# Performance work log

Hardware: AMD Instinct MI355X
Metric: run time of the kernel (lower is better)

The kernel has to match this reference:

```python
import jax, jax.numpy as jnp
import numpy as np

V = 6890      # FAUST vertex count (also n_classes)
R, A = 5, 8   # radial / angular template discretization
C_IN = 544    # SHOT descriptor dim
DIMS = [96, 128, 128]  # isc_layer_dims


def setup_inputs() -> dict:
    key = jax.random.key(0)
    ks = jax.random.split(key, 12)
    signal = jax.random.normal(ks[0], (V, C_IN), jnp.float32)
    bc_idx = jax.random.randint(ks[1], (V, R, A, 3), 0, V, jnp.int32)
    w = jax.random.uniform(ks[2], (V, R, A, 3), jnp.float32)
    bc_w = w / jnp.sum(w, axis=-1, keepdims=True)  # barycentric weights sum to 1
    c_ins = [C_IN] + DIMS[:-1]
    params = {}
    for i, (t, c) in enumerate(zip(DIMS, c_ins)):
        params[f"t{i}"] = jax.random.normal(ks[3 + 2 * i], (t, R, A, c), jnp.float32) * 0.05
        params[f"b{i}"] = jnp.zeros((t,), jnp.float32)
    Wd = jax.random.normal(ks[10], (DIMS[-1], V), jnp.float32) * 0.05
    bd = jnp.zeros((V,), jnp.float32)
    return {"signal": signal, "bc_idx": bc_idx, "bc_w": bc_w, **params, "Wd": Wd, "bd": bd}


def _conv_dirac_amp(sig, idx, w, T, b):
    # barycentric interpolation of the signal at template vertices:
    # gather sig[idx] -> [V,R,A,3,C], weight-sum over the 3 corners -> [V,R,A,C]
    interp = jnp.einsum('vrai,vraic->vrac', w, sig[idx])
    # template matching for every angular rotation (rotation_delta=1 -> A rotations)
    outs = [jnp.einsum('vrac,trac->vt', jnp.roll(interp, -o, axis=2), T) for o in range(A)]
    x = jax.nn.relu(jnp.stack(outs, axis=1) + b)  # [V, A_rot, T]
    # AngularMaxPooling: max over rotation axis
    return jnp.max(x, axis=1)  # [V, T]


def reference(signal, bc_idx, bc_w, t0, b0, t1, b1, t2, b2, Wd, bd):
    x = signal
    for T, b in ((t0, b0), (t1, b1), (t2, b2)):
        x = _conv_dirac_amp(x, bc_idx, bc_w, T, b)
    return x @ Wd + bd  # [V, 6890] per-vertex class logits
```

## Files before the change

kernel.cpp:

```cpp
#include <hip/hip_runtime.h>

typedef unsigned short u16;
typedef unsigned int   u32;
typedef __bf16 bf16x8 __attribute__((ext_vector_type(8)));
typedef float  f32x4  __attribute__((ext_vector_type(4)));
typedef u32    u32x4  __attribute__((ext_vector_type(4)));
typedef u32    u32x2  __attribute__((ext_vector_type(2)));
typedef u16    u16x4  __attribute__((ext_vector_type(4)));

#define V_N   6890
#define V_PAD 6912
#define SQ2H  0.70710678118654752f

__device__ __forceinline__ float bf2f(u32 h) {
  union { u32 u; float f; } c; c.u = h << 16; return c.f;
}
__device__ __forceinline__ u16 f2bf(float f) {
  union { float f; u32 u; } c; c.f = f;
  return (u16)((c.u + 0x7fffu + ((c.u >> 16) & 1u)) >> 16);
}
__device__ __forceinline__ u32 pk(float lo, float hi) {
  return (u32)f2bf(lo) | ((u32)f2bf(hi) << 16);
}
__device__ __forceinline__ void gload_lds16(const void* g, void* l) {
  __builtin_amdgcn_global_load_lds((const __attribute__((address_space(1))) void*)g,
                                   (__attribute__((address_space(3))) void*)l, 16, 0, 0);
}

__device__ __forceinline__ void rfft8(const float* x, float& Z0, float& Re1, float& Im1,
                                      float& Re2, float& Im2, float& Re3, float& Im3, float& Z4) {
  float s04 = x[0] + x[4], d04 = x[0] - x[4];
  float s26 = x[2] + x[6], d26 = x[2] - x[6];
  float s15 = x[1] + x[5], d15 = x[1] - x[5];
  float s37 = x[3] + x[7], d37 = x[3] - x[7];
  float e = s04 + s26, f = s15 + s37;
  Z0 = e + f; Z4 = e - f;
  Re2 = s04 - s26; Im2 = s37 - s15;
  float t1 = SQ2H * (d15 - d37), t2 = SQ2H * (d15 + d37);
  Re1 = d04 + t1; Re3 = d04 - t1;
  Im1 = -(t2 + d26); Im3 = d26 - t2;
}

__global__ void cvt_kernel(const float* __restrict__ in, u16* __restrict__ out, int total4) {
  int g = blockIdx.x * 256 + threadIdx.x;
  if (g >= total4) return;
  f32x4 v = *(const f32x4*)(in + (size_t)g * 4);
  u16x4 o; o.x = f2bf(v.x); o.y = f2bf(v.y); o.z = f2bf(v.z); o.w = f2bf(v.w);
  *(u16x4*)(out + (size_t)g * 4) = o;
}

__global__ void trot_fft_kernel(const float* __restrict__ T, u16* __restrict__ B,
                                int Tn, int Cc, int C4, int K0pad, int K1, int total) {
  int g = blockIdx.x * 256 + threadIdx.x;
  if (g >= total) return;
  int c4 = g % C4; int q = g / C4;
  int r = q % 5; int t = q / 5;
  float hs[8][4];
#pragma unroll
  for (int a = 0; a < 8; ++a) {
    f32x4 va = *(const f32x4*)(T + ((size_t)((t * 5 + r) * 8 + a)) * Cc + c4 * 4);
#pragma unroll
    for (int j = 0; j < 4; ++j) hs[a][j] = va[j];
  }
  float Z0[4], Z4[4], Re[3][4], Im[3][4];
#pragma unroll
  for (int ch = 0; ch < 4; ++ch) {
    float x[8];
#pragma unroll
    for (int a = 0; a < 8; ++a) x[a] = hs[a][ch];
    float z0, r1, i1, r2, i2, r3, i3, z4;
    rfft8(x, z0, r1, i1, r2, i2, r3, i3, z4);
    Z0[ch] = z0 * 0.125f; Z4[ch] = z4 * 0.125f;
    Re[0][ch] = r1 * 0.25f; Im[0][ch] = i1 * 0.25f;
    Re[1][ch] = r2 * 0.25f; Im[1][ch] = i2 * 0.25f;
    Re[2][ch] = r3 * 0.25f; Im[2][ch] = i3 * 0.25f;
  }
  int cb = c4 * 4;
  u32x2 w0v; w0v[0] = pk(Z0[0], Z0[1]); w0v[1] = pk(Z0[2], Z0[3]);
  *(u32x2*)(B + (size_t)t * K0pad + r * Cc + cb) = w0v;
  size_t bo1 = (size_t)Tn * K0pad;
  size_t binSz = (size_t)2 * Tn * K1;
  int off = ((r * Cc + cb) << 1);
#pragma unroll
  for (int k = 0; k < 3; ++k) {
    u32x4 wr, wi;
#pragma unroll
    for (int j = 0; j < 4; ++j) {
      wr[j] = pk(Re[k][j], Im[k][j]);
      wi[j] = pk(-Im[k][j], Re[k][j]);
    }
    *(u32x4*)(B + bo1 + k * binSz + (size_t)t * K1 + off) = wr;
    *(u32x4*)(B + bo1 + k * binSz + (size_t)(Tn + t) * K1 + off) = wi;
  }
  u32x2 w4v; w4v[0] = pk(Z4[0], Z4[1]); w4v[1] = pk(Z4[2], Z4[3]);
  *(u32x2*)(B + bo1 + 3 * binSz + (size_t)t * K0pad + r * Cc + cb) = w4v;
}

__global__ void bpad_kernel(u16* __restrict__ B, int K0pad, int pad, size_t b4off, int total) {
  int g = blockIdx.x * 256 + threadIdx.x;
  if (g >= total) return;
  int p = g % pad; int t = g / pad;
  size_t o = (size_t)t * K0pad + (K0pad - pad) + p;
  B[o] = 0;
  B[b4off + o] = 0;
}

__global__ void interp_fft_kernel(const u16* __restrict__ sig, int Cc, int C8,
                                  const int* __restrict__ idx, const float* __restrict__ wgt,
                                  u16* __restrict__ out, int v0, int Kpad, int K0pad, int K1,
                                  int total) {
  int g = blockIdx.x * 256 + threadIdx.x;
  if (g >= total) return;
  int c8 = g % C8; int q = g / C8;
  int r = q % 5; int vr = q / 5;
  size_t ib = ((size_t)((v0 + vr) * 5 + r)) * 24;
  float xs[8][8];
#pragma unroll
  for (int a = 0; a < 8; ++a) {
    int i0 = idx[ib + a * 3], i1 = idx[ib + a * 3 + 1], i2 = idx[ib + a * 3 + 2];
    float w0 = wgt[ib + a * 3], w1 = wgt[ib + a * 3 + 1], w2 = wgt[ib + a * 3 + 2];
    u32x4 s0 = *(const u32x4*)(sig + (size_t)i0 * Cc + c8 * 8);
    u32x4 s1 = *(const u32x4*)(sig + (size_t)i1 * Cc + c8 * 8);
    u32x4 s2 = *(const u32x4*)(sig + (size_t)i2 * Cc + c8 * 8);
#pragma unroll
    for (int j = 0; j < 4; ++j) {
      xs[a][2 * j]     = w0 * bf2f(s0[j] & 0xffffu) + w1 * bf2f(s1[j] & 0xffffu) + w2 * bf2f(s2[j] & 0xffffu);
      xs[a][2 * j + 1] = w0 * bf2f(s0[j] >> 16)     + w1 * bf2f(s1[j] >> 16)     + w2 * bf2f(s2[j] >> 16);
    }
  }
  float Z0[8], Z4[8], Re1[8], Im1[8], Re2[8], Im2[8], Re3[8], Im3[8];
#pragma unroll
  for (int ch = 0; ch < 8; ++ch) {
    float x[8];
#pragma unroll
    for (int a = 0; a < 8; ++a) x[a] = xs[a][ch];
    rfft8(x, Z0[ch], Re1[ch], Im1[ch], Re2[ch], Im2[ch], Re3[ch], Im3[ch], Z4[ch]);
  }
  size_t rowb = (size_t)vr * Kpad;
  int cb = c8 * 8;
  u32x4 a0, a4;
#pragma unroll
  for (int p = 0; p < 4; ++p) {
    a0[p] = pk(Z0[2 * p], Z0[2 * p + 1]);
    a4[p] = pk(Z4[2 * p], Z4[2 * p + 1]);
  }
  *(u32x4*)(out + rowb + r * Cc + cb) = a0;
  *(u32x4*)(out + rowb + K0pad + 3 * K1 + r * Cc + cb) = a4;
  int off1 = K0pad + ((r * Cc + cb) << 1);
  u32x4 wa, wb;
#pragma unroll
  for (int j = 0; j < 4; ++j) { wa[j] = pk(Re1[j], Im1[j]); wb[j] = pk(Re1[4 + j], Im1[4 + j]); }
  *(u32x4*)(out + rowb + off1) = wa;
  *(u32x4*)(out + rowb + off1 + 8) = wb;
#pragma unroll
  for (int j = 0; j < 4; ++j) { wa[j] = pk(Re2[j], Im2[j]); wb[j] = pk(Re2[4 + j], Im2[4 + j]); }
  *(u32x4*)(out + rowb + off1 + K1) = wa;
  *(u32x4*)(out + rowb + off1 + K1 + 8) = wb;
#pragma unroll
  for (int j = 0; j < 4; ++j) { wa[j] = pk(Re3[j], Im3[j]); wb[j] = pk(Re3[4 + j], Im3[4 + j]); }
  *(u32x4*)(out + rowb + off1 + 2 * K1) = wa;
  *(u32x4*)(out + rowb + off1 + 2 * K1 + 8) = wb;
}

__global__ void amp_fft(const float* __restrict__ Cin, size_t cstride,
                        const float* __restrict__ bias, u16* __restrict__ out,
                        int Tn, int ldo, int split,
                        int ns0, int ns1, int ns2, int ns3, int ns4, int total) {
  int g = blockIdx.x * 256 + threadIdx.x;
  if (g >= total) return;
  int t = g % Tn, v = g / Tn;
  const int nsA[8] = {ns0, ns1, ns1, ns2, ns2, ns3, ns3, ns4};
  float sec[8];
  size_t base = (size_t)v * (8 * Tn) + t;
#pragma unroll
  for (int s = 0; s < 8; ++s) {
    const float* p = Cin + base + s * Tn;
    float a = p[0];
    for (int k = 1; k < nsA[s]; ++k) a += p[(size_t)k * cstride];
    sec[s] = a;
  }
  const float Ct[8] = {1.f, SQ2H, 0.f, -SQ2H, -1.f, -SQ2H, 0.f, SQ2H};
  const float St[8] = {0.f, SQ2H, 1.f, SQ2H, 0.f, -SQ2H, -1.f, -SQ2H};
  float m;
#pragma unroll
  for (int o = 0; o < 8; ++o) {
    float val = sec[0] + ((o & 1) ? -sec[7] : sec[7])
      + sec[1] * Ct[o]           - sec[2] * St[o]
      + sec[3] * Ct[(2 * o) & 7] - sec[4] * St[(2 * o) & 7]
      + sec[5] * Ct[(3 * o) & 7] - sec[6] * St[(3 * o) & 7];
    m = (o == 0) ? val : fmaxf(m, val);
  }
  m = fmaxf(m + bias[t], 0.f);
  u16 hi = f2bf(m);
  out[(size_t)v * ldo + t] = hi;
  if (split) out[(size_t)v * ldo + Tn + t] = f2bf(m - bf2f(hi));
}

__global__ void wdt_kernel(const float* __restrict__ Wd, u16* __restrict__ out, int total) {
  int g = blockIdx.x * 256 + threadIdx.x;
  if (g >= total) return;
  int k = g & 127, n = g >> 7;
  float v = (n < V_N) ? Wd[(size_t)k * V_N + n] : 0.f;
  u16 hi = f2bf(v);
  out[(size_t)n * 256 + k] = hi;
  out[(size_t)n * 256 + 128 + k] = f2bf(v - bf2f(hi));
}

struct GTab {
  int start[6];
  int aOff[5];
  int bOff[5];
  int cOff[5];
  int Kg[5];
  int kch[5];
  int ntn[5];
  int Nv[5];
};

__global__ __launch_bounds__(512, 2) void gemm_grp(
    const u16* __restrict__ A, int lda, const u16* __restrict__ Bbase,
    float* __restrict__ C, int ldc, size_t cstride,
    const float* __restrict__ bias, int Mvalid, int ntm, int nG, GTab tb) {
  __shared__ __align__(16) u16 lA[2][256 * 64];
  __shared__ __align__(16) u16 lB[2][256 * 64];
  const int tid = threadIdx.x;
  const int w = tid >> 6, l = tid & 63;

  const int nb = gridDim.x, bid = blockIdx.x;
  const int qq = nb >> 3, rr = nb & 7;
  const int xcd = bid & 7, ii = bid >> 3;
  const int vb = (xcd < rr ? xcd * (qq + 1) : rr * (qq + 1) + (xcd - rr) * qq) + ii;

  int gI = 0;
#pragma unroll
  for (int k = 1; k < 5; ++k) if (k < nG && vb >= tb.start[k]) gI = k;
  const int local = vb - tb.start[gI];
  const int ntnG = tb.ntn[gI];
  const int per = ntm * ntnG;
  const int s = local / per;
  const int rem = local - s * per;
  const int tm = rem / ntnG, tn = rem - tm * ntnG;
  const int Kg = tb.Kg[gI];
  const int kb = s * tb.kch[gI];
  int ke = kb + tb.kch[gI]; if (ke > Kg) ke = Kg;
  const int nt = (ke - kb + 63) >> 6;
  const int Nv = tb.Nv[gI];
  const int cO = tb.cOff[gI];
  const int ldb = Kg;
  float* Cb = C + (size_t)s * cstride;

  const u16* Ab = A + (size_t)(tm * 256) * lda + tb.aOff[gI] + kb;
  const u16* Bb = Bbase + tb.bOff[gI] + (size_t)(tn * 256) * ldb + kb;

  const int srow = tid >> 3;
  const int scol = (((l & 7) ^ (srow & 7)) << 3);
  u16* laBase = &lA[0][0];
  u16* lbBase = &lB[0][0];

  auto STAGE = [&](int buf, int k0) {
    const u16* ga = Ab + (size_t)srow * lda + k0 + scol;
    const u16* gb = Bb + (size_t)srow * ldb + k0 + scol;
    u16* la = laBase + buf * (256 * 64) + w * 512;
    u16* lb = lbBase + buf * (256 * 64) + w * 512;
#pragma unroll
    for (int i = 0; i < 4; ++i) {
      gload_lds16(ga + (size_t)(i * 64) * lda, la + i * 4096);
      gload_lds16(gb + (size_t)(i * 64) * ldb, lb + i * 4096);
    }
  };

  f32x4 acc[8][4];
#pragma unroll
  for (int i = 0; i < 8; ++i)
#pragma unroll
    for (int j = 0; j < 4; ++j) acc[i][j] = (f32x4){0.f, 0.f, 0.f, 0.f};

  const int wm = w >> 2, wn = w & 3;
  const int aoffbase = (wm * 128 + (l & 15)) * 64;
  const int boffbase = (wn * 64 + (l & 15)) * 64;
  const int ksel = l >> 4, swz = l & 7;
  const int kc0 = ((ksel ^ swz) << 3);
  const int kc1 = (((4 + ksel) ^ swz) << 3);

  STAGE(0, 0);
  int cur = 0;
  for (int t = 0; t < nt; ++t) {
    if (t + 1 < nt) STAGE(cur ^ 1, (t + 1) * 64);
    __builtin_amdgcn_sched_barrier(0);
    if (t + 1 < nt) { asm volatile("s_waitcnt vmcnt(8)" ::: "memory"); }
    else            { asm volatile("s_waitcnt vmcnt(0)" ::: "memory"); }
    __builtin_amdgcn_s_barrier();
    __builtin_amdgcn_sched_barrier(0);
    const u16* lab = laBase + cur * (256 * 64);
    const u16* lbb = lbBase + cur * (256 * 64);
#pragma unroll
    for (int kk = 0; kk < 2; ++kk) {
      const int kc = kk ? kc1 : kc0;
      bf16x8 bfr[4];
#pragma unroll
      for (int ni = 0; ni < 4; ++ni)
        bfr[ni] = *(const bf16x8*)&lbb[boffbase + ni * 1024 + kc];
#pragma unroll
      for (int mh = 0; mh < 2; ++mh) {
        bf16x8 afr[4];
#pragma unroll
        for (int mi = 0; mi < 4; ++mi)
          afr[mi] = *(const bf16x8*)&lab[aoffbase + (mh * 4 + mi) * 1024 + kc];
        __builtin_amdgcn_s_setprio(1);
#pragma unroll
        for (int mi = 0; mi < 4; ++mi)
#pragma unroll
          for (int ni = 0; ni < 4; ++ni)
            acc[mh * 4 + mi][ni] =
                __builtin_amdgcn_mfma_f32_16x16x32_bf16(afr[mi], bfr[ni], acc[mh * 4 + mi][ni], 0, 0, 0);
        __builtin_amdgcn_s_setprio(0);
      }
    }
    __builtin_amdgcn_sched_barrier(0);
    __builtin_amdgcn_s_barrier();
    cur ^= 1;
  }

  const int row0 = tm * 256 + wm * 128 + ((l >> 4) << 2);
  const int col0 = tn * 256 + wn * 64 + (l & 15);
#pragma unroll
  for (int mi = 0; mi < 8; ++mi) {
#pragma unroll
    for (int j = 0; j < 4; ++j) {
      int grow = row0 + mi * 16 + j;
      if (grow < Mvalid) {
#pragma unroll
        for (int ni = 0; ni < 4; ++ni) {
          int gcol = col0 + ni * 16;
          if (gcol < Nv) {
            float vv = acc[mi][ni][j];
            int gc = cO + gcol;
            if (bias) vv += bias[gc];
            Cb[(size_t)grow * ldc + gc] = vv;
          }
        }
      }
    }
  }
}

static inline int imin(int a, int b) { return a < b ? a : b; }

extern "C" void kernel_launch(void* const* d_in, const int* in_sizes, int n_in,
                              void* d_out, int out_size, void* d_ws, size_t ws_size,
                              hipStream_t stream) {
  const float* signal = (const float*)d_in[0];
  const int*   bc_idx = (const int*)d_in[1];
  const float* bc_w   = (const float*)d_in[2];
  const float* tmpl[3] = { (const float*)d_in[3], (const float*)d_in[5], (const float*)d_in[7] };
  const float* tb[3]   = { (const float*)d_in[4], (const float*)d_in[6], (const float*)d_in[8] };
  const float* Wd = (const float*)d_in[9];
  const float* bd = (const float*)d_in[10];
  float* outp = (float*)d_out;

  char* ws = (char*)d_ws;
  size_t off = 0;
  auto alloc = [&](size_t b) -> void* {
    size_t o = (off + 255) & ~(size_t)255; off = o + b; return (void*)(ws + o);
  };
  u16* sigbf = (u16*)alloc((size_t)V_N * 544 * 2);
  u16* outL0 = (u16*)alloc((size_t)V_PAD * 96 * 2);
  u16* outL1 = (u16*)alloc((size_t)V_PAD * 128 * 2);
  u16* outL2 = (u16*)alloc((size_t)V_PAD * 256 * 2);
  u16* trot  = (u16*)alloc((size_t)8 * 1024 * 1024 * 2);
  float* gemmC = (float*)alloc((size_t)4 * V_PAD * 1024 * 4);
  size_t o2 = (off + 255) & ~(size_t)255;
  u16* interp = (u16*)(ws + o2);
  size_t interpElems = (ws_size > o2) ? (ws_size - o2) / 2 : 0;

  { int total4 = V_N * 544 / 4;
    cvt_kernel<<<dim3((total4 + 255) / 256), dim3(256), 0, stream>>>(signal, sigbf, total4); }

  const int TnA[3] = {96, 128, 128}, CcA[3] = {544, 96, 128};
  const int nsTab[3][5] = {{2,5,5,4,2},{3,4,4,4,3},{3,4,4,4,3}};
  const int CrA[3] = {3584, V_PAD, V_PAD};
  u16* outs[3] = { outL0, outL1, outL2 };
  const u16* cursig = sigbf;
  for (int L = 0; L < 3; ++L) {
    const int Tn = TnA[L], Cc = CcA[L];
    const int C8 = Cc / 8, C4 = Cc / 4;
    const int K0 = 5 * Cc, K0pad = ((K0 + 63) / 64) * 64;
    const int K1 = 10 * Cc;
    const int Kpad = 2 * K0pad + 3 * K1;
    const int N = 8 * Tn;
    const int* ns = nsTab[L];
    const size_t cstride = (size_t)V_PAD * N;

    { int total = Tn * 5 * C4;
      trot_fft_kernel<<<dim3((total + 255) / 256), dim3(256), 0, stream>>>(
          tmpl[L], trot, Tn, Cc, C4, K0pad, K1, total); }
    int pad = K0pad - K0;
    if (pad > 0) {
      int total = Tn * pad;
      size_t b4off = (size_t)Tn * K0pad + (size_t)6 * Tn * K1;
      bpad_kernel<<<dim3((total + 255) / 256), dim3(256), 0, stream>>>(trot, K0pad, pad, b4off, total);
    }

    GTab tg;
    int Kg5[5] = {K0pad, K1, K1, K1, K0pad};
    int Ng5[5] = {Tn, 2 * Tn, 2 * Tn, 2 * Tn, Tn};
    tg.aOff[0] = 0; tg.aOff[1] = K0pad; tg.aOff[2] = K0pad + K1;
    tg.aOff[3] = K0pad + 2 * K1; tg.aOff[4] = K0pad + 3 * K1;
    tg.bOff[0] = 0; tg.bOff[1] = Tn * K0pad;
    tg.bOff[2] = Tn * K0pad + 2 * Tn * K1;
    tg.bOff[3] = Tn * K0pad + 4 * Tn * K1;
    tg.bOff[4] = Tn * K0pad + 6 * Tn * K1;
    tg.cOff[0] = 0; tg.cOff[1] = Tn; tg.cOff[2] = 3 * Tn; tg.cOff[3] = 5 * Tn; tg.cOff[4] = 7 * Tn;
    for (int g5 = 0; g5 < 5; ++g5) {
      tg.Kg[g5] = Kg5[g5];
      tg.kch[g5] = ((Kg5[g5] / 64 + ns[g5] - 1) / ns[g5]) * 64;
      tg.ntn[g5] = 1;
      tg.Nv[g5] = Ng5[g5];
    }

    long crl = (long)(interpElems / (size_t)Kpad) & ~(long)255;
    int cr = (crl > (long)CrA[L]) ? CrA[L] : (int)crl;
    if (cr < 256) cr = 256;
    for (int v0 = 0; v0 < V_PAD; v0 += cr) {
      int rows = imin(cr, V_PAD - v0);
      int nv = imin(rows, V_N - v0);
      { int total = nv * 5 * C8;
        interp_fft_kernel<<<dim3((total + 255) / 256), dim3(256), 0, stream>>>(
            cursig, Cc, C8, bc_idx, bc_w, interp, v0, Kpad, K0pad, K1, total); }
      int ntm = rows / 256;
      tg.start[0] = 0;
      for (int g5 = 0; g5 < 5; ++g5) tg.start[g5 + 1] = tg.start[g5] + ns[g5] * ntm;
      gemm_grp<<<dim3(tg.start[5]), dim3(512), 0, stream>>>(
          interp, Kpad, trot, gemmC + (size_t)v0 * N, N, cstride, nullptr, nv, ntm, 5, tg);
    }
    { int total = V_N * Tn;
      int ldo = (L == 2) ? 256 : ((L == 0) ? 96 : 128);
      amp_fft<<<dim3((total + 255) / 256), dim3(256), 0, stream>>>(
          gemmC, cstride, tb[L], outs[L], Tn, ldo, (L == 2) ? 1 : 0,
          ns[0], ns[1], ns[2], ns[3], ns[4], total); }
    cursig = outs[L];
  }

  { int total = V_PAD * 128;
    wdt_kernel<<<dim3((total + 255) / 256), dim3(256), 0, stream>>>(Wd, trot, total); }
  GTab td;
  td.start[0] = 0; td.start[1] = 27 * 27;
  td.aOff[0] = 0; td.bOff[0] = 0; td.cOff[0] = 0;
  td.Kg[0] = 256; td.kch[0] = 256; td.ntn[0] = 27; td.Nv[0] = V_N;
  for (int g5 = 1; g5 < 5; ++g5) { td.start[g5 + 1] = td.start[1]; td.aOff[g5] = 0; td.bOff[g5] = 0;
    td.cOff[g5] = 0; td.Kg[g5] = 256; td.kch[g5] = 256; td.ntn[g5] = 1; td.Nv[g5] = 0; }
  gemm_grp<<<dim3(27 * 27), dim3(512), 0, stream>>>(
      outL2, 256, trot, outp, V_N, 0, bd, V_N, 27, 1, td);
}
```

Baseline: 637.8 us.

## Add half-width N tile for real-bin GEMM groups, cut split-K, fuse pad kernel

Adds a 256x128 tile variant to the grouped GEMM for the DC and Nyquist bins, whose N is only Tn (96 or 128), so half of the old 256-wide B tile is no longer wasted. The split-K factors for layers 1 and 2 are lowered, which reduces partial-sum output traffic and the reduction work in amp_fft. The bpad zeroing kernel is folded into the trot FFT kernel to save one launch per layer. In exchange there are fewer blocks in layers 1 and 2 and more branching in the GEMM kernel, which may raise register pressure.

```diff
diff --git a/kernel.cpp b/kernel.cpp
--- a/kernel.cpp
+++ b/kernel.cpp
@@ -50,9 +50,18 @@
 }
 
 __global__ void trot_fft_kernel(const float* __restrict__ T, u16* __restrict__ B,
-                                int Tn, int Cc, int C4, int K0pad, int K1, int total) {
+                                int Tn, int Cc, int C4, int K0pad, int K1, int total, int pad) {
   int g = blockIdx.x * 256 + threadIdx.x;
-  if (g >= total) return;
+  if (g >= total) {
+    int g2 = g - total;
+    int padTot = Tn * pad;
+    if (g2 >= padTot) return;
+    int p = g2 % pad; int t = g2 / pad;
+    size_t b4off = (size_t)Tn * K0pad + (size_t)6 * Tn * K1;
+    size_t o = (size_t)t * K0pad + (K0pad - pad) + p;
+    B[o] = 0; B[b4off + o] = 0;
+    return;
+  }
   int c4 = g % C4; int q = g / C4;
   int r = q % 5; int t = q / 5;
   float hs[8][4];
@@ -94,15 +103,6 @@
   }
   u32x2 w4v; w4v[0] = pk(Z4[0], Z4[1]); w4v[1] = pk(Z4[2], Z4[3]);
   *(u32x2*)(B + bo1 + 3 * binSz + (size_t)t * K0pad + r * Cc + cb) = w4v;
-}
-
-__global__ void bpad_kernel(u16* __restrict__ B, int K0pad, int pad, size_t b4off, int total) {
-  int g = blockIdx.x * 256 + threadIdx.x;
-  if (g >= total) return;
-  int p = g % pad; int t = g / pad;
-  size_t o = (size_t)t * K0pad + (K0pad - pad) + p;
-  B[o] = 0;
-  B[b4off + o] = 0;
 }
 
 __global__ void interp_fft_kernel(const u16* __restrict__ sig, int Cc, int C8,
@@ -215,6 +215,7 @@
   int kch[5];
   int ntn[5];
   int Nv[5];
+  int nh[5];
 };
 
 __global__ __launch_bounds__(512, 2) void gemm_grp(
@@ -246,97 +247,170 @@
   const int nt = (ke - kb + 63) >> 6;
   const int Nv = tb.Nv[gI];
   const int cO = tb.cOff[gI];
+  const int nh = tb.nh[gI];
   const int ldb = Kg;
   float* Cb = C + (size_t)s * cstride;
 
   const u16* Ab = A + (size_t)(tm * 256) * lda + tb.aOff[gI] + kb;
-  const u16* Bb = Bbase + tb.bOff[gI] + (size_t)(tn * 256) * ldb + kb;
+  const u16* Bb = Bbase + tb.bOff[gI] + (size_t)(tn * (nh ? 128 : 256)) * ldb + kb;
 
   const int srow = tid >> 3;
   const int scol = (((l & 7) ^ (srow & 7)) << 3);
   u16* laBase = &lA[0][0];
   u16* lbBase = &lB[0][0];
 
-  auto STAGE = [&](int buf, int k0) {
-    const u16* ga = Ab + (size_t)srow * lda + k0 + scol;
-    const u16* gb = Bb + (size_t)srow * ldb + k0 + scol;
-    u16* la = laBase + buf * (256 * 64) + w * 512;
-    u16* lb = lbBase + buf * (256 * 64) + w * 512;
-#pragma unroll
-    for (int i = 0; i < 4; ++i) {
-      gload_lds16(ga + (size_t)(i * 64) * lda, la + i * 4096);
-      gload_lds16(gb + (size_t)(i * 64) * ldb, lb + i * 4096);
-    }
-  };
-
   f32x4 acc[8][4];
 #pragma unroll
   for (int i = 0; i < 8; ++i)
 #pragma unroll
     for (int j = 0; j < 4; ++j) acc[i][j] = (f32x4){0.f, 0.f, 0.f, 0.f};
 
-  const int wm = w >> 2, wn = w & 3;
-  const int aoffbase = (wm * 128 + (l & 15)) * 64;
-  const int boffbase = (wn * 64 + (l & 15)) * 64;
   const int ksel = l >> 4, swz = l & 7;
   const int kc0 = ((ksel ^ swz) << 3);
   const int kc1 = (((4 + ksel) ^ swz) << 3);
 
-  STAGE(0, 0);
-  int cur = 0;
-  for (int t = 0; t < nt; ++t) {
-    if (t + 1 < nt) STAGE(cur ^ 1, (t + 1) * 64);
-    __builtin_amdgcn_sched_barrier(0);
-    if (t + 1 < nt) { asm volatile("s_waitcnt vmcnt(8)" ::: "memory"); }
-    else            { asm volatile("s_waitcnt vmcnt(0)" ::: "memory"); }
-    __builtin_amdgcn_s_barrier();
-    __builtin_amdgcn_sched_barrier(0);
-    const u16* lab = laBase + cur * (256 * 64);
-    const u16* lbb = lbBase + cur * (256 * 64);
-#pragma unroll
-    for (int kk = 0; kk < 2; ++kk) {
-      const int kc = kk ? kc1 : kc0;
-      bf16x8 bfr[4];
-#pragma unroll
-      for (int ni = 0; ni < 4; ++ni)
-        bfr[ni] = *(const bf16x8*)&lbb[boffbase + ni * 1024 + kc];
-#pragma unroll
-      for (int mh = 0; mh < 2; ++mh) {
+  if (nh) {
+    const int wm = w >> 1, wn = w & 1;
+    const int aoffbase = (wm * 64 + (l & 15)) * 64;
+    const int boffbase = (wn * 64 + (l & 15)) * 64;
+    auto STAGE = [&](int buf, int k0) {
+      const u16* ga = Ab + (size_t)srow * lda + k0 + scol;
+      const u16* gb = Bb + (size_t)srow * ldb + k0 + scol;
+      u16* la = laBase + buf * (256 * 64) + w * 512;
+      u16* lb = lbBase + buf * (256 * 64) + w * 512;
+#pragma unroll
+      for (int i = 0; i < 4; ++i)
+        gload_lds16(ga + (size_t)(i * 64) * lda, la + i * 4096);
+#pragma unroll
+      for (int i = 0; i < 2; ++i)
+        gload_lds16(gb + (size_t)(i * 64) * ldb, lb + i * 4096);
+    };
+    STAGE(0, 0);
+    int cur = 0;
+    for (int t = 0; t < nt; ++t) {
+      if (t + 1 < nt) STAGE(cur ^ 1, (t + 1) * 64);
+      __builtin_amdgcn_sched_barrier(0);
+      if (t + 1 < nt) { asm volatile("s_waitcnt vmcnt(6)" ::: "memory"); }
+      else            { asm volatile("s_waitcnt vmcnt(0)" ::: "memory"); }
+      __builtin_amdgcn_s_barrier();
+      __builtin_amdgcn_sched_barrier(0);
+      const u16* lab = laBase + cur * (256 * 64);
+      const u16* lbb = lbBase + cur * (256 * 64);
+#pragma unroll
+      for (int kk = 0; kk < 2; ++kk) {
+        const int kc = kk ? kc1 : kc0;
+        bf16x8 bfr[4];
+#pragma unroll
+        for (int ni = 0; ni < 4; ++ni)
+          bfr[ni] = *(const bf16x8*)&lbb[boffbase + ni * 1024 + kc];
         bf16x8 afr[4];
 #pragma unroll
         for (int mi = 0; mi < 4; ++mi)
-          afr[mi] = *(const bf16x8*)&lab[aoffbase + (mh * 4 + mi) * 1024 + kc];
+          afr[mi] = *(const bf16x8*)&lab[aoffbase + mi * 1024 + kc];
         __builtin_amdgcn_s_setprio(1);
 #pragma unroll
         for (int mi = 0; mi < 4; ++mi)
 #pragma unroll
           for (int ni = 0; ni < 4; ++ni)
-            acc[mh * 4 + mi][ni] =
-                __builtin_amdgcn_mfma_f32_16x16x32_bf16(afr[mi], bfr[ni], acc[mh * 4 + mi][ni], 0, 0, 0);
+            acc[mi][ni] =
+                __builtin_amdgcn_mfma_f32_16x16x32_bf16(afr[mi], bfr[ni], acc[mi][ni], 0, 0, 0);
         __builtin_amdgcn_s_setprio(0);
       }
-    }
-    __builtin_amdgcn_sched_barrier(0);
-    __builtin_amdgcn_s_barrier();
-    cur ^= 1;
-  }
-
-  const int row0 = tm * 256 + wm * 128 + ((l >> 4) << 2);
-  const int col0 = tn * 256 + wn * 64 + (l & 15);
-#pragma unroll
-  for (int mi = 0; mi < 8; ++mi) {
-#pragma unroll
-    for (int j = 0; j < 4; ++j) {
-      int grow = row0 + mi * 16 + j;
-      if (grow < Mvalid) {
-#pragma unroll
-        for (int ni = 0; ni < 4; ++ni) {
-          int gcol = col0 + ni * 16;
-          if (gcol < Nv) {
-            float vv = acc[mi][ni][j];
-            int gc = cO + gcol;
-            if (bias) vv += bias[gc];
-            Cb[(size_t)grow * ldc + gc] = vv;
+      __builtin_amdgcn_sched_barrier(0);
+      __builtin_amdgcn_s_barrier();
+      cur ^= 1;
+    }
+    const int row0 = tm * 256 + wm * 64 + ((l >> 4) << 2);
+    const int col0 = tn * 128 + wn * 64 + (l & 15);
+#pragma unroll
+    for (int mi = 0; mi < 4; ++mi) {
+#pragma unroll
+      for (int j = 0; j < 4; ++j) {
+        int grow = row0 + mi * 16 + j;
+        if (grow < Mvalid) {
+#pragma unroll
+          for (int ni = 0; ni < 4; ++ni) {
+            int gcol = col0 + ni * 16;
+            if (gcol < Nv) {
+              float vv = acc[mi][ni][j];
+              int gc = cO + gcol;
+              if (bias) vv += bias[gc];
+              Cb[(size_t)grow * ldc + gc] = vv;
+            }
+          }
+        }
+      }
+    }
+  } else {
+    const int wm = w >> 2, wn = w & 3;
+    const int aoffbase = (wm * 128 + (l & 15)) * 64;
+    const int boffbase = (wn * 64 + (l & 15)) * 64;
+    auto STAGE = [&](int buf, int k0) {
+      const u16* ga = Ab + (size_t)srow * lda + k0 + scol;
+      const u16* gb = Bb + (size_t)srow * ldb + k0 + scol;
+      u16* la = laBase + buf * (256 * 64) + w * 512;
+      u16* lb = lbBase + buf * (256 * 64) + w * 512;
+#pragma unroll
+      for (int i = 0; i < 4; ++i) {
+        gload_lds16(ga + (size_t)(i * 64) * lda, la + i * 4096);
+        gload_lds16(gb + (size_t)(i * 64) * ldb, lb + i * 4096);
+      }
+    };
+    STAGE(0, 0);
+    int cur = 0;
+    for (int t = 0; t < nt; ++t) {
+      if (t + 1 < nt) STAGE(cur ^ 1, (t + 1) * 64);
+      __builtin_amdgcn_sched_barrier(0);
+      if (t + 1 < nt) { asm volatile("s_waitcnt vmcnt(8)" ::: "memory"); }
+      else            { asm volatile("s_waitcnt vmcnt(0)" ::: "memory"); }
+      __builtin_amdgcn_s_barrier();
+      __builtin_amdgcn_sched_barrier(0);
+      const u16* lab = laBase + cur * (256 * 64);
+      const u16* lbb = lbBase + cur * (256 * 64);
+#pragma unroll
+      for (int kk = 0; kk < 2; ++kk) {
+        const int kc = kk ? kc1 : kc0;
+        bf16x8 bfr[4];
+#pragma unroll
+        for (int ni = 0; ni < 4; ++ni)
+          bfr[ni] = *(const bf16x8*)&lbb[boffbase + ni * 1024 + kc];
+#pragma unroll
+        for (int mh = 0; mh < 2; ++mh) {
+          bf16x8 afr[4];
+#pragma unroll
+          for (int mi = 0; mi < 4; ++mi)
+            afr[mi] = *(const bf16x8*)&lab[aoffbase + (mh * 4 + mi) * 1024 + kc];
+          __builtin_amdgcn_s_setprio(1);
+#pragma unroll
+          for (int mi = 0; mi < 4; ++mi)
+#pragma unroll
+            for (int ni = 0; ni < 4; ++ni)
+              acc[mh * 4 + mi][ni] =
+                  __builtin_amdgcn_mfma_f32_16x16x32_bf16(afr[mi], bfr[ni], acc[mh * 4 + mi][ni], 0, 0, 0);
+          __builtin_amdgcn_s_setprio(0);
+        }
+      }
+      __builtin_amdgcn_sched_barrier(0);
+      __builtin_amdgcn_s_barrier();
+      cur ^= 1;
+    }
+    const int row0 = tm * 256 + wm * 128 + ((l >> 4) << 2);
+    const int col0 = tn * 256 + wn * 64 + (l & 15);
+#pragma unroll
+    for (int mi = 0; mi < 8; ++mi) {
+#pragma unroll
+      for (int j = 0; j < 4; ++j) {
+        int grow = row0 + mi * 16 + j;
+        if (grow < Mvalid) {
+#pragma unroll
+          for (int ni = 0; ni < 4; ++ni) {
+            int gcol = col0 + ni * 16;
+            if (gcol < Nv) {
+              float vv = acc[mi][ni][j];
+              int gc = cO + gcol;
+              if (bias) vv += bias[gc];
+              Cb[(size_t)grow * ldc + gc] = vv;
+            }
           }
         }
       }
@@ -377,7 +451,7 @@
     cvt_kernel<<<dim3((total4 + 255) / 256), dim3(256), 0, stream>>>(signal, sigbf, total4); }
 
   const int TnA[3] = {96, 128, 128}, CcA[3] = {544, 96, 128};
-  const int nsTab[3][5] = {{2,5,5,4,2},{3,4,4,4,3},{3,4,4,4,3}};
+  const int nsTab[3][5] = {{2,5,5,4,2},{1,2,2,2,1},{1,2,2,2,1}};
   const int CrA[3] = {3584, V_PAD, V_PAD};
   u16* outs[3] = { outL0, outL1, outL2 };
   const u16* cursig = sigbf;
@@ -390,16 +464,12 @@
     const int N = 8 * Tn;
     const int* ns = nsTab[L];
     const size_t cstride = (size_t)V_PAD * N;
+    const int pad = K0pad - K0;
 
     { int total = Tn * 5 * C4;
-      trot_fft_kernel<<<dim3((total + 255) / 256), dim3(256), 0, stream>>>(
-          tmpl[L], trot, Tn, Cc, C4, K0pad, K1, total); }
-    int pad = K0pad - K0;
-    if (pad > 0) {
-      int total = Tn * pad;
-      size_t b4off = (size_t)Tn * K0pad + (size_t)6 * Tn * K1;
-      bpad_kernel<<<dim3((total + 255) / 256), dim3(256), 0, stream>>>(trot, K0pad, pad, b4off, total);
-    }
+      int total2 = total + Tn * pad;
+      trot_fft_kernel<<<dim3((total2 + 255) / 256), dim3(256), 0, stream>>>(
+          tmpl[L], trot, Tn, Cc, C4, K0pad, K1, total, pad); }
 
     GTab tg;
     int Kg5[5] = {K0pad, K1, K1, K1, K0pad};
@@ -416,6 +486,7 @@
       tg.kch[g5] = ((Kg5[g5] / 64 + ns[g5] - 1) / ns[g5]) * 64;
       tg.ntn[g5] = 1;
       tg.Nv[g5] = Ng5[g5];
+      tg.nh[g5] = (g5 == 0 || g5 == 4) ? 1 : 0;
     }
 
     long crl = (long)(interpElems / (size_t)Kpad) & ~(long)255;
@@ -446,9 +517,9 @@
   GTab td;
   td.start[0] = 0; td.start[1] = 27 * 27;
   td.aOff[0] = 0; td.bOff[0] = 0; td.cOff[0] = 0;
-  td.Kg[0] = 256; td.kch[0] = 256; td.ntn[0] = 27; td.Nv[0] = V_N;
+  td.Kg[0] = 256; td.kch[0] = 256; td.ntn[0] = 27; td.Nv[0] = V_N; td.nh[0] = 0;
   for (int g5 = 1; g5 < 5; ++g5) { td.start[g5 + 1] = td.start[1]; td.aOff[g5] = 0; td.bOff[g5] = 0;
-    td.cOff[g5] = 0; td.Kg[g5] = 256; td.kch[g5] = 256; td.ntn[g5] = 1; td.Nv[g5] = 0; }
+    td.cOff[g5] = 0; td.Kg[g5] = 256; td.kch[g5] = 256; td.ntn[g5] = 1; td.Nv[g5] = 0; td.nh[g5] = 0; }
   gemm_grp<<<dim3(27 * 27), dim3(512), 0, stream>>>(
       outL2, 256, trot, outp, V_N, 0, bd, V_N, 27, 1, td);
 }
```

After: 563.9 us. 1.13x faster.
